# Kernel optimization log

Hardware: AMD Instinct MI355X
Metric: run time of the kernel (lower is better)

Reference implementation:

```python
import jax, jax.numpy as jnp
import numpy as np

N, E, H, OUT, NTYPES, EDGE_IN, T = 20000, 160000, 64, 3, 9, 4, 3
NODE_IN = OUT + 1 + NTYPES  # normalized velocity + normalized youngs + one-hot node type


def _mlp(x, w1, b1, w2, b2):
    # 2-layer MLP with ReLU hidden activation (encoder/processor/decoder blocks)
    return jnp.dot(jax.nn.relu(jnp.dot(x, w1) + b1), w2) + b2


def setup_inputs() -> dict:
    key = jax.random.key(0)
    ks = iter(jax.random.split(key, 48))
    nrm = lambda shape, s=1.0: jax.random.normal(next(ks), shape, jnp.float32) * s
    W = 0.05  # small init scale keeps RK4 trajectories numerically tame
    inp = {
        'world_pos': nrm((N, 3)),
        'velocity': nrm((N, 3)) * 0.1,
        'edge_index': jax.random.randint(next(ks), (2, E), 0, N),
        'mesh_edge_attr': nrm((E, EDGE_IN)),
        'youngs': jax.random.uniform(next(ks), (N, 1), jnp.float32) + 0.5,
        'one_hot_node_type': jax.nn.one_hot(jax.random.randint(next(ks), (N,), 0, NTYPES), NTYPES, dtype=jnp.float32),
        'node_type': jax.random.randint(next(ks), (N, 1), 0, 3),
        't_span': jnp.arange(T, dtype=jnp.float32) * 0.1,  # rk4 step_size=0.1 -> one step per interval
        # normalization statistics (stats dict in the torch code)
        'youngs_mean': jnp.full((1,), 1.0, jnp.float32), 'youngs_std': jnp.ones((1,), jnp.float32),
        'mesh_edge_mean': nrm((EDGE_IN,)) * 0.1, 'mesh_edge_std': jnp.ones((EDGE_IN,), jnp.float32),
        'vel_mean': nrm((3,)) * 0.01, 'vel_std': jnp.ones((3,), jnp.float32),
        'acc_mean': nrm((3,)) * 0.01, 'acc_std': jnp.ones((3,), jnp.float32),
        # node encoder
        'w_ne1': nrm((NODE_IN, H), W), 'b_ne1': jnp.zeros((H,), jnp.float32),
        'w_ne2': nrm((H, H), W), 'b_ne2': jnp.zeros((H,), jnp.float32),
        # edge encoder
        'w_ee1': nrm((EDGE_IN, H), W), 'b_ee1': jnp.zeros((H,), jnp.float32),
        'w_ee2': nrm((H, H), W), 'b_ee2': jnp.zeros((H,), jnp.float32),
        # processor edge-update MLP (in: [e, h_src, h_dst])
        'w_em1': nrm((3 * H, H), W), 'b_em1': jnp.zeros((H,), jnp.float32),
        'w_em2': nrm((H, H), W), 'b_em2': jnp.zeros((H,), jnp.float32),
        # processor node-update MLP (in: [h, agg])
        'w_nm1': nrm((2 * H, H), W), 'b_nm1': jnp.zeros((H,), jnp.float32),
        'w_nm2': nrm((H, H), W), 'b_nm2': jnp.zeros((H,), jnp.float32),
        # decoder -> acceleration
        'w_dec1': nrm((H, H), W), 'b_dec1': jnp.zeros((H,), jnp.float32),
        'w_dec2': nrm((H, OUT), W), 'b_dec2': jnp.zeros((OUT,), jnp.float32),
    }
    return inp


def reference(world_pos, velocity, edge_index, mesh_edge_attr, youngs, one_hot_node_type, node_type, t_span,
              youngs_mean, youngs_std, mesh_edge_mean, mesh_edge_std, vel_mean, vel_std, acc_mean, acc_std,
              w_ne1, b_ne1, w_ne2, b_ne2, w_ee1, b_ee1, w_ee2, b_ee2,
              w_em1, b_em1, w_em2, b_em2, w_nm1, b_nm1, w_nm2, b_nm2,
              w_dec1, b_dec1, w_dec2, b_dec2):
    n = world_pos.shape[0]
    other = jnp.concatenate([(youngs - youngs_mean) / youngs_std, one_hot_node_type], axis=-1)  # [N, 10]
    eattr = (mesh_edge_attr - mesh_edge_mean) / mesh_edge_std  # [E, 4] static, normalized once
    src, dst = edge_index[0], edge_index[1]

    def deriv(pos, vel):
        # NeuralODEFunc: encode -> message passing -> decode acceleration
        vn = (vel - vel_mean) / vel_std
        h = _mlp(jnp.concatenate([vn, other], axis=-1), w_ne1, b_ne1, w_ne2, b_ne2)  # [N, H]
        e = _mlp(eattr, w_ee1, b_ee1, w_ee2, b_ee2)  # [E, H]
        # residual GraphNet block: gather endpoint features, update edges, scatter-sum to nodes
        e = e + _mlp(jnp.concatenate([e, h[src], h[dst]], axis=-1), w_em1, b_em1, w_em2, b_em2)
        agg = jax.ops.segment_sum(e, dst, num_segments=n)  # [N, H]
        h = h + _mlp(jnp.concatenate([h, agg], axis=-1), w_nm1, b_nm1, w_nm2, b_nm2)
        acc = _mlp(h, w_dec1, b_dec1, w_dec2, b_dec2) * acc_std + acc_mean  # unnormalize
        return vel, acc  # d(pos)/dt, d(vel)/dt

    def rk4_step(state, dt):
        pos, vel = state
        k1p, k1v = deriv(pos, vel)
        k2p, k2v = deriv(pos + 0.5 * dt * k1p, vel + 0.5 * dt * k1v)
        k3p, k3v = deriv(pos + 0.5 * dt * k2p, vel + 0.5 * dt * k2v)
        k4p, k4v = deriv(pos + dt * k3p, vel + dt * k3v)
        sixth = dt / 6.0
        pos = pos + sixth * (k1p + 2.0 * k2p + 2.0 * k3p + k4p)
        vel = vel + sixth * (k1v + 2.0 * k2v + 2.0 * k3v + k4v)
        return (pos, vel), (pos, vel)

    dts = t_span[1:] - t_span[:-1]  # equals rk4 step_size 0.1 -> one step per interval
    _, (ptraj, vtraj) = jax.lax.scan(rk4_step, (world_pos, velocity), dts)
    pos_out = jnp.concatenate([world_pos[None], ptraj], axis=0)  # [T, N, 3]
    vel_out = jnp.concatenate([velocity[None], vtraj], axis=0)  # [T, N, 3]
    return pos_out, vel_out
```

## Files before the change

### kernel.cpp

```cpp
#include <hip/hip_runtime.h>
#include <hip/hip_bf16.h>

#define NN 20000
#define NE 160000
#define HD 64
#define TT 3

typedef unsigned short ushortx8 __attribute__((ext_vector_type(8)));
typedef float f32x4 __attribute__((ext_vector_type(4)));
typedef __bf16 bf16x8 __attribute__((ext_vector_type(8)));

__device__ __forceinline__ unsigned short f2bf(float f) {
  unsigned int x = __float_as_uint(f);
  unsigned int r = (x + 0x7fffu + ((x >> 16) & 1u)) >> 16;
  return (unsigned short)r;
}
__device__ __forceinline__ float bf2f(unsigned short u) {
  return __uint_as_float(((unsigned int)u) << 16);
}

__global__ __launch_bounds__(256) void k_prep(const float* __restrict__ wp,
    const float* __restrict__ vel, float* __restrict__ PO, float* __restrict__ VO,
    int* __restrict__ counts, int* __restrict__ fill,
    const float* __restrict__ youngs, const float* __restrict__ onehot,
    const float* __restrict__ ym, const float* __restrict__ ys,
    const float* __restrict__ w_ne1, const float* __restrict__ b_ne1, float* __restrict__ h_pre,
    const float* __restrict__ w_em1, const float* __restrict__ w_em2,
    const float* __restrict__ w_nm1, const float* __restrict__ w_nm2,
    const float* __restrict__ w_dec1, const float* __restrict__ w_ne2, const float* __restrict__ w_ee2,
    char* __restrict__ w1em, char* __restrict__ w2em, char* __restrict__ wnm1,
    char* __restrict__ wnm2, char* __restrict__ wdec1, char* __restrict__ wne2,
    char* __restrict__ wee2) {
  int idx = blockIdx.x * 256 + threadIdx.x;
  if (idx < NN * 3) { PO[idx] = wp[idx]; VO[idx] = vel[idx]; }
  if (idx < NN) { counts[idx] = 0; fill[idx] = 0; }
  {
    int n = idx >> 6, j = idx & 63;
    float a = b_ne1[j];
    float yn = (youngs[n] - ym[0]) / ys[0];
    a += yn * w_ne1[3 * HD + j];
#pragma unroll
    for (int k = 0; k < 9; k++) a += onehot[n * 9 + k] * w_ne1[(4 + k) * HD + j];
    h_pre[idx] = a;
  }
  int w = idx;
  if (w < 12288) {
    int j = w / 192, k = w % 192;
    *(unsigned short*)(w1em + j * 384 + ((k * 2) ^ ((j & 7) << 4))) = f2bf(w_em1[k * 64 + j]);
    return;
  }
  w -= 12288;
  if (w < 4096) {
    int j = w >> 6, k = w & 63;
    *(unsigned short*)(w2em + j * 128 + ((k * 2) ^ ((j & 7) << 4))) = f2bf(w_em2[k * 64 + j]);
    return;
  }
  w -= 4096;
  if (w < 8192) {
    int j = w >> 7, k = w & 127;
    *(unsigned short*)(wnm1 + j * 256 + ((k * 2) ^ ((j & 7) << 4))) = f2bf(w_nm1[k * 64 + j]);
    return;
  }
  w -= 8192;
  if (w < 4096) {
    int j = w >> 6, k = w & 63;
    *(unsigned short*)(wnm2 + j * 128 + ((k * 2) ^ ((j & 7) << 4))) = f2bf(w_nm2[k * 64 + j]);
    return;
  }
  w -= 4096;
  if (w < 4096) {
    int j = w >> 6, k = w & 63;
    *(unsigned short*)(wdec1 + j * 128 + ((k * 2) ^ ((j & 7) << 4))) = f2bf(w_dec1[k * 64 + j]);
    return;
  }
  w -= 4096;
  if (w < 4096) {
    int j = w >> 6, k = w & 63;
    *(unsigned short*)(wne2 + j * 128 + ((k * 2) ^ ((j & 7) << 4))) = f2bf(w_ne2[k * 64 + j]);
    return;
  }
  w -= 4096;
  if (w < 4096) {
    int j = w >> 6, k = w & 63;
    *(unsigned short*)(wee2 + j * 128 + ((k * 2) ^ ((j & 7) << 4))) = f2bf(w_ee2[k * 64 + j]);
    return;
  }
}

__global__ __launch_bounds__(256) void k_edge_enc_mfma(const float* __restrict__ eattr,
    const float* __restrict__ emean, const float* __restrict__ estd,
    const float* __restrict__ w_ee1, const float* __restrict__ b_ee1,
    const char* __restrict__ wee2sw, const float* __restrict__ b_ee2,
    char* __restrict__ eenc_sw) {
  __shared__ __align__(16) char s_w2[64 * 128];
  __shared__ __align__(16) char s_hid[64 * 128];
  __shared__ float s_w1[4 * 64], s_b1[64], s_b2[64], s_m[4], s_s[4];
  int tid = threadIdx.x, e0b = blockIdx.x * 64;
  for (int c = tid; c < 512; c += 256) ((ushortx8*)s_w2)[c] = ((const ushortx8*)wee2sw)[c];
  if (tid < 256) s_w1[tid] = w_ee1[tid];
  if (tid < 64) { s_b1[tid] = b_ee1[tid]; s_b2[tid] = b_ee2[tid]; }
  if (tid < 4) { s_m[tid] = emean[tid]; s_s[tid] = estd[tid]; }
  __syncthreads();
  int lane = tid & 63, wv = tid >> 6, l15 = lane & 15, lq = lane >> 4, csub = lq * 8;
  int row_l = wv * 16 + l15, rsw = (l15 & 7) << 4;
  int erow = e0b + row_l;
  float4 at = ((const float4*)eattr)[erow];
  float x0 = (at.x - s_m[0]) / s_s[0];
  float x1 = (at.y - s_m[1]) / s_s[1];
  float x2 = (at.z - s_m[2]) / s_s[2];
  float x3 = (at.w - s_m[3]) / s_s[3];
#pragma unroll 4
  for (int i = 0; i < 16; i++) {
    int rl = wv * 16 + i;
    float y0 = __shfl(x0, i), y1 = __shfl(x1, i), y2 = __shfl(x2, i), y3 = __shfl(x3, i);
    float a = s_b1[lane] + y0 * s_w1[lane] + y1 * s_w1[64 + lane] + y2 * s_w1[128 + lane] + y3 * s_w1[192 + lane];
    *(unsigned short*)(s_hid + rl * 128 + ((lane * 2) ^ ((rl & 7) << 4))) = f2bf(fmaxf(a, 0.f));
  }
  f32x4 acc[4];
#pragma unroll
  for (int n = 0; n < 4; n++) {
    float bv = s_b2[n * 16 + l15];
#pragma unroll
    for (int i = 0; i < 4; i++) acc[n][i] = bv;
  }
#pragma unroll
  for (int kk = 0; kk < 2; kk++) {
    ushortx8 au = *(const ushortx8*)(s_hid + row_l * 128 + (((kk * 32 + csub) * 2) ^ rsw));
    bf16x8 av = __builtin_bit_cast(bf16x8, au);
#pragma unroll
    for (int n = 0; n < 4; n++) {
      int j = n * 16 + l15;
      ushortx8 bu = *(const ushortx8*)(s_w2 + j * 128 + (((kk * 32 + csub) * 2) ^ ((j & 7) << 4)));
      acc[n] = __builtin_amdgcn_mfma_f32_16x16x32_bf16(av, __builtin_bit_cast(bf16x8, bu), acc[n], 0, 0, 0);
    }
  }
#pragma unroll
  for (int n = 0; n < 4; n++) {
#pragma unroll
    for (int i = 0; i < 4; i++) {
      int r = wv * 16 + lq * 4 + i, col = n * 16 + l15;
      *(unsigned short*)(s_hid + r * 128 + ((col * 2) ^ ((r & 7) << 4))) = f2bf(acc[n][i]);
    }
  }
  ushortx8 q0 = *(const ushortx8*)(s_hid + row_l * 128 + lq * 32);
  ushortx8 q1 = *(const ushortx8*)(s_hid + row_l * 128 + lq * 32 + 16);
  *(ushortx8*)(eenc_sw + (size_t)erow * 128 + lq * 32) = q0;
  *(ushortx8*)(eenc_sw + (size_t)erow * 128 + lq * 32 + 16) = q1;
}

__global__ __launch_bounds__(256) void k_count(const int* __restrict__ eidx, int* __restrict__ counts) {
  int e = blockIdx.x * 256 + threadIdx.x;
  if (e < NE) atomicAdd(&counts[eidx[NE + e]], 1);
}

#define SCAN_NB ((NN + 255) / 256)
__global__ __launch_bounds__(256) void k_scanA(const int* __restrict__ counts,
    int* __restrict__ row_ptr, int* __restrict__ bsums) {
  __shared__ int tmp[256];
  int tid = threadIdx.x;
  int g = blockIdx.x * 256 + tid;
  int v = (g < NN) ? counts[g] : 0;
  tmp[tid] = v;
  __syncthreads();
#pragma unroll
  for (int off = 1; off < 256; off <<= 1) {
    int t = (tid >= off) ? tmp[tid - off] : 0;
    __syncthreads();
    tmp[tid] += t;
    __syncthreads();
  }
  if (g < NN) row_ptr[g] = tmp[tid] - v;
  if (tid == 255) bsums[blockIdx.x] = tmp[255];
}

__global__ __launch_bounds__(128) void k_scanB(int* __restrict__ bsums) {
  __shared__ int tmp[128];
  int tid = threadIdx.x;
  int v = (tid < SCAN_NB) ? bsums[tid] : 0;
  tmp[tid] = v;
  __syncthreads();
#pragma unroll
  for (int off = 1; off < 128; off <<= 1) {
    int t = (tid >= off) ? tmp[tid - off] : 0;
    __syncthreads();
    tmp[tid] += t;
    __syncthreads();
  }
  if (tid < SCAN_NB) bsums[tid] = tmp[tid] - v;
}

__global__ __launch_bounds__(256) void k_scanC(int* __restrict__ row_ptr, const int* __restrict__ bsums) {
  int g = blockIdx.x * 256 + threadIdx.x;
  if (g < NN) row_ptr[g] += bsums[blockIdx.x];
  if (g == 0) row_ptr[NN] = NE;
}

__global__ __launch_bounds__(256) void k_place(const int* __restrict__ eidx,
    const int* __restrict__ row_ptr, int* __restrict__ fill, int* __restrict__ slot) {
  int e = blockIdx.x * 256 + threadIdx.x;
  if (e >= NE) return;
  int d = eidx[NE + e];
  int f = atomicAdd(&fill[d], 1);
  slot[e] = row_ptr[d] + f;
}

__global__ __launch_bounds__(256) void k_enc_mfma(const float* __restrict__ vel,
    const float* __restrict__ vmean, const float* __restrict__ vstd,
    const float* __restrict__ w_ne1, const float* __restrict__ h_pre,
    const char* __restrict__ wne2sw, const float* __restrict__ b_ne2,
    float* __restrict__ h, unsigned short* __restrict__ h_bf) {
  __shared__ __align__(16) char s_w2[64 * 128];
  __shared__ __align__(16) char s_hid[64 * 128];
  __shared__ float s_w1[3 * 64], s_b2[64], s_vm[3], s_vs[3];
  int tid = threadIdx.x, n0b = blockIdx.x * 64;
  for (int c = tid; c < 512; c += 256) ((ushortx8*)s_w2)[c] = ((const ushortx8*)wne2sw)[c];
  if (tid < 192) s_w1[tid] = w_ne1[tid];
  if (tid < 64) s_b2[tid] = b_ne2[tid];
  if (tid < 3) { s_vm[tid] = vmean[tid]; s_vs[tid] = vstd[tid]; }
  __syncthreads();
  int lane = tid & 63, wv = tid >> 6, l15 = lane & 15, lq = lane >> 4, csub = lq * 8;
#pragma unroll 4
  for (int i = 0; i < 16; i++) {
    int rl = wv * 16 + i, node = n0b + rl;
    float hv = 0.f;
    if (node < NN) {
      float v0 = (vel[node * 3 + 0] - s_vm[0]) / s_vs[0];
      float v1 = (vel[node * 3 + 1] - s_vm[1]) / s_vs[1];
      float v2 = (vel[node * 3 + 2] - s_vm[2]) / s_vs[2];
      float a = h_pre[(size_t)node * 64 + lane] + v0 * s_w1[lane] + v1 * s_w1[64 + lane] + v2 * s_w1[128 + lane];
      hv = fmaxf(a, 0.f);
    }
    *(unsigned short*)(s_hid + rl * 128 + ((lane * 2) ^ ((rl & 7) << 4))) = f2bf(hv);
  }
  int row_l = wv * 16 + l15, rsw = (l15 & 7) << 4;
  f32x4 acc[4];
#pragma unroll
  for (int n = 0; n < 4; n++) {
    float bv = s_b2[n * 16 + l15];
#pragma unroll
    for (int i = 0; i < 4; i++) acc[n][i] = bv;
  }
#pragma unroll
  for (int kk = 0; kk < 2; kk++) {
    ushortx8 au = *(const ushortx8*)(s_hid + row_l * 128 + (((kk * 32 + csub) * 2) ^ rsw));
    bf16x8 av = __builtin_bit_cast(bf16x8, au);
#pragma unroll
    for (int n = 0; n < 4; n++) {
      int j = n * 16 + l15;
      ushortx8 bu = *(const ushortx8*)(s_w2 + j * 128 + (((kk * 32 + csub) * 2) ^ ((j & 7) << 4)));
      acc[n] = __builtin_amdgcn_mfma_f32_16x16x32_bf16(av, __builtin_bit_cast(bf16x8, bu), acc[n], 0, 0, 0);
    }
  }
#pragma unroll
  for (int n = 0; n < 4; n++) {
#pragma unroll
    for (int i = 0; i < 4; i++) {
      int r = wv * 16 + lq * 4 + i, rowg = n0b + r, col = n * 16 + l15;
      if (rowg < NN) h[(size_t)rowg * 64 + col] = acc[n][i];
      *(unsigned short*)(s_hid + r * 128 + ((col * 2) ^ ((r & 7) << 4))) = f2bf(acc[n][i]);
    }
  }
  int noderow = n0b + row_l;
  if (noderow < NN) {
    ushortx8 q0 = *(const ushortx8*)(s_hid + row_l * 128 + ((lq * 32) ^ rsw));
    ushortx8 q1 = *(const ushortx8*)(s_hid + row_l * 128 + ((lq * 32 + 16) ^ rsw));
    ushortx8* op = (ushortx8*)(h_bf + (size_t)noderow * 64);
    op[lq * 2] = q0;
    op[lq * 2 + 1] = q1;
  }
}

#define EDGE_GRID 1024
__global__ __launch_bounds__(256, 4) void k_edge_mfma(
    const int* __restrict__ eidx, const int* __restrict__ slot,
    const unsigned short* __restrict__ h_bf, const char* __restrict__ eenc_sw,
    const char* __restrict__ w1sw, const char* __restrict__ w2sw,
    const float* __restrict__ b_em1, const float* __restrict__ b_em2,
    unsigned short* __restrict__ emsg) {
  __shared__ __align__(16) char s_w1[64 * 384];
  __shared__ __align__(16) char s_w2[64 * 128];
  __shared__ __align__(16) char s_eh[64 * 128];
  int tid = threadIdx.x;
  int lane = tid & 63, wv = tid >> 6, l15 = lane & 15, lq = lane >> 4, csub = lq * 8;
  int erow_loc = wv * 16 + l15;
  int rsw = (l15 & 7) << 4;
  for (int c = tid; c < 1536; c += 256) ((ushortx8*)s_w1)[c] = ((const ushortx8*)w1sw)[c];
  for (int c = tid; c < 512; c += 256) ((ushortx8*)s_w2)[c] = ((const ushortx8*)w2sw)[c];
  float bv1[4], bv2[4];
#pragma unroll
  for (int n = 0; n < 4; n++) { bv1[n] = b_em1[n * 16 + l15]; bv2[n] = b_em2[n * 16 + l15]; }

  const int NT = NE / 64;
  ushortx8 stg0, stg1;
  {
    const ushortx8* src = (const ushortx8*)(eenc_sw + (size_t)blockIdx.x * 64 * 128);
    stg0 = src[tid];
    stg1 = src[tid + 256];
  }
  for (int t = blockIdx.x; t < NT; t += EDGE_GRID) {
    int e0b = t * 64;
    int eg = e0b + erow_loc;
    int sidx = eidx[eg], didx = eidx[NE + eg], sl = slot[eg];
    const ushortx8* hs = (const ushortx8*)(h_bf + (size_t)sidx * HD);
    const ushortx8* hd = (const ushortx8*)(h_bf + (size_t)didx * HD);
    ushortx8 a2 = hs[lq];
    ushortx8 a3 = hs[4 + lq];
    ushortx8 a4 = hd[lq];
    ushortx8 a5 = hd[4 + lq];
    __syncthreads();
    ((ushortx8*)s_eh)[tid] = stg0;
    ((ushortx8*)s_eh)[tid + 256] = stg1;
    __syncthreads();
    int tn = t + EDGE_GRID;
    if (tn < NT) {
      const ushortx8* srcn = (const ushortx8*)(eenc_sw + (size_t)tn * 64 * 128);
      stg0 = srcn[tid];
      stg1 = srcn[tid + 256];
    }
    ushortx8 a0 = *(const ushortx8*)(s_eh + erow_loc * 128 + ((csub * 2) ^ rsw));
    ushortx8 a1 = *(const ushortx8*)(s_eh + erow_loc * 128 + ((64 + csub * 2) ^ rsw));
    f32x4 acc[4];
#pragma unroll
    for (int n = 0; n < 4; n++) {
#pragma unroll
      for (int i = 0; i < 4; i++) acc[n][i] = bv1[n];
    }
    ushortx8 af[6] = {a0, a1, a2, a3, a4, a5};
#pragma unroll
    for (int kk = 0; kk < 6; kk++) {
      bf16x8 av = __builtin_bit_cast(bf16x8, af[kk]);
#pragma unroll
      for (int n = 0; n < 4; n++) {
        int j = n * 16 + l15;
        ushortx8 bu = *(const ushortx8*)(s_w1 + j * 384 + (((kk * 32 + csub) * 2) ^ ((j & 7) << 4)));
        acc[n] = __builtin_amdgcn_mfma_f32_16x16x32_bf16(av, __builtin_bit_cast(bf16x8, bu), acc[n], 0, 0, 0);
      }
    }
    f32x4 acc2[4];
#pragma unroll
    for (int n = 0; n < 4; n++) {
#pragma unroll
      for (int i = 0; i < 4; i++) {
        int r = wv * 16 + lq * 4 + i, col = n * 16 + l15;
        unsigned short ev = *(const unsigned short*)(s_eh + r * 128 + ((col * 2) ^ ((r & 7) << 4)));
        acc2[n][i] = bv2[n] + bf2f(ev);
      }
    }
#pragma unroll
    for (int n = 0; n < 4; n++) {
#pragma unroll
      for (int i = 0; i < 4; i++) {
        int r = wv * 16 + lq * 4 + i, col = n * 16 + l15;
        *(unsigned short*)(s_eh + r * 128 + ((col * 2) ^ ((r & 7) << 4))) = f2bf(fmaxf(acc[n][i], 0.f));
      }
    }
#pragma unroll
    for (int kk = 0; kk < 2; kk++) {
      ushortx8 au = *(const ushortx8*)(s_eh + erow_loc * 128 + (((kk * 32 + csub) * 2) ^ rsw));
      bf16x8 av = __builtin_bit_cast(bf16x8, au);
#pragma unroll
      for (int n = 0; n < 4; n++) {
        int j = n * 16 + l15;
        ushortx8 bu = *(const ushortx8*)(s_w2 + j * 128 + (((kk * 32 + csub) * 2) ^ ((j & 7) << 4)));
        acc2[n] = __builtin_amdgcn_mfma_f32_16x16x32_bf16(av, __builtin_bit_cast(bf16x8, bu), acc2[n], 0, 0, 0);
      }
    }
#pragma unroll
    for (int n = 0; n < 4; n++) {
#pragma unroll
      for (int i = 0; i < 4; i++) {
        int r = wv * 16 + lq * 4 + i, col = n * 16 + l15;
        *(unsigned short*)(s_eh + r * 128 + ((col * 2) ^ ((r & 7) << 4))) = f2bf(acc2[n][i]);
      }
    }
    ushortx8 q0 = *(const ushortx8*)(s_eh + erow_loc * 128 + ((lq * 32) ^ rsw));
    ushortx8 q1 = *(const ushortx8*)(s_eh + erow_loc * 128 + ((lq * 32 + 16) ^ rsw));
    ushortx8* op = (ushortx8*)(emsg + (size_t)sl * HD);
    op[lq * 2] = q0;
    op[lq * 2 + 1] = q1;
  }
}

__global__ __launch_bounds__(128) void k_upd_enc(
    const int* __restrict__ row_ptr, const unsigned short* __restrict__ emsg,
    float* __restrict__ hbuf, unsigned short* __restrict__ h_bf,
    const char* __restrict__ wnm1sw, const char* __restrict__ wnm2sw,
    const char* __restrict__ wdec1sw, const char* __restrict__ wne2sw,
    const float* __restrict__ b_nm1, const float* __restrict__ b_nm2,
    const float* __restrict__ b_dec1, const float* __restrict__ b_dec2,
    const float* __restrict__ w_dec2, const float* __restrict__ amean, const float* __restrict__ astd,
    const float* __restrict__ w_ne1, const float* __restrict__ h_pre,
    const float* __restrict__ b_ne2, const float* __restrict__ vmean, const float* __restrict__ vstd,
    const float* __restrict__ tspan, int s, int k, int do_enc,
    const float* __restrict__ V0, float* __restrict__ vacc, float* __restrict__ pacc,
    const float* __restrict__ pos_prev, float* __restrict__ pos_next, float* __restrict__ vel_next) {
  __shared__ __align__(16) char s_w1[64 * 256];
  __shared__ __align__(16) char s_w2[64 * 128];
  __shared__ __align__(16) char s_wd1[64 * 128];
  __shared__ __align__(16) char s_w2e[64 * 128];
  __shared__ __align__(16) char s_ah[32 * 128];
  __shared__ float s_b1[64], s_b2[64], s_bd1[64], s_be2[64], s_wd2[192], s_w1e[192];
  __shared__ float s_vm[3], s_vs[3];
  int tid = threadIdx.x, n0b = blockIdx.x * 32;
  for (int c = tid; c < 1024; c += 128) ((ushortx8*)s_w1)[c] = ((const ushortx8*)wnm1sw)[c];
  for (int c = tid; c < 512; c += 128) ((ushortx8*)s_w2)[c] = ((const ushortx8*)wnm2sw)[c];
  for (int c = tid; c < 512; c += 128) ((ushortx8*)s_wd1)[c] = ((const ushortx8*)wdec1sw)[c];
  for (int c = tid; c < 512; c += 128) ((ushortx8*)s_w2e)[c] = ((const ushortx8*)wne2sw)[c];
  if (tid < 64) { s_b1[tid] = b_nm1[tid]; s_b2[tid] = b_nm2[tid]; s_bd1[tid] = b_dec1[tid]; s_be2[tid] = b_ne2[tid]; }
  for (int i = tid; i < 192; i += 128) { s_wd2[i] = w_dec2[i]; s_w1e[i] = w_ne1[i]; }
  if (tid < 3) { s_vm[tid] = vmean[tid]; s_vs[tid] = vstd[tid]; }

  int lane = tid & 63, wv = tid >> 6, l15 = lane & 15, lq = lane >> 4, csub = lq * 8;
  int row_l = wv * 16 + l15, rsw = (l15 & 7) << 4;
  int noderow = n0b + row_l;
  int ncl = noderow < NN ? noderow : NN - 1;
  ushortx8 afh0 = *(const ushortx8*)(h_bf + (size_t)ncl * 64 + csub);
  ushortx8 afh1 = *(const ushortx8*)(h_bf + (size_t)ncl * 64 + 32 + csub);

  int arow = lane >> 3, ag = lane & 7;
#pragma unroll
  for (int p = 0; p < 2; p++) {
    int rl = wv * 16 + p * 8 + arow, node = n0b + rl;
    float sm[8] = {0.f, 0.f, 0.f, 0.f, 0.f, 0.f, 0.f, 0.f};
    if (node < NN) {
      int b = row_ptr[node], e = row_ptr[node + 1];
      for (int r = b; r < e; r++) {
        ushortx8 u = *(const ushortx8*)(emsg + (size_t)r * HD + ag * 8);
#pragma unroll
        for (int j = 0; j < 8; j++) sm[j] += bf2f(u[j]);
      }
    }
    ushortx8 u;
#pragma unroll
    for (int j = 0; j < 8; j++) u[j] = f2bf(sm[j]);
    *(ushortx8*)(s_ah + rl * 128 + ((ag * 16) ^ ((rl & 7) << 4))) = u;
  }
  __syncthreads();

  f32x4 acc[4];
#pragma unroll
  for (int n = 0; n < 4; n++) {
    float bv = s_b1[n * 16 + l15];
#pragma unroll
    for (int i = 0; i < 4; i++) acc[n][i] = bv;
  }
  ushortx8 af[4];
  af[0] = afh0; af[1] = afh1;
  af[2] = *(const ushortx8*)(s_ah + row_l * 128 + ((csub * 2) ^ rsw));
  af[3] = *(const ushortx8*)(s_ah + row_l * 128 + (((32 + csub) * 2) ^ rsw));
#pragma unroll
  for (int kk = 0; kk < 4; kk++) {
    bf16x8 av = __builtin_bit_cast(bf16x8, af[kk]);
#pragma unroll
    for (int n = 0; n < 4; n++) {
      int j = n * 16 + l15;
      ushortx8 bu = *(const ushortx8*)(s_w1 + j * 256 + (((kk * 32 + csub) * 2) ^ ((j & 7) << 4)));
      acc[n] = __builtin_amdgcn_mfma_f32_16x16x32_bf16(av, __builtin_bit_cast(bf16x8, bu), acc[n], 0, 0, 0);
    }
  }
#pragma unroll
  for (int n = 0; n < 4; n++) {
#pragma unroll
    for (int i = 0; i < 4; i++) {
      int r = wv * 16 + lq * 4 + i, col = n * 16 + l15;
      *(unsigned short*)(s_ah + r * 128 + ((col * 2) ^ ((r & 7) << 4))) = f2bf(fmaxf(acc[n][i], 0.f));
    }
  }
  f32x4 acc2[4];
#pragma unroll
  for (int n = 0; n < 4; n++) {
#pragma unroll
    for (int i = 0; i < 4; i++) {
      int r = wv * 16 + lq * 4 + i, col = n * 16 + l15;
      int rg = n0b + r; int rgc = rg < NN ? rg : NN - 1;
      acc2[n][i] = s_b2[col] + hbuf[(size_t)rgc * 64 + col];
    }
  }
#pragma unroll
  for (int kk = 0; kk < 2; kk++) {
    ushortx8 au = *(const ushortx8*)(s_ah + row_l * 128 + (((kk * 32 + csub) * 2) ^ rsw));
    bf16x8 av = __builtin_bit_cast(bf16x8, au);
#pragma unroll
    for (int n = 0; n < 4; n++) {
      int j = n * 16 + l15;
      ushortx8 bu = *(const ushortx8*)(s_w2 + j * 128 + (((kk * 32 + csub) * 2) ^ ((j & 7) << 4)));
      acc2[n] = __builtin_amdgcn_mfma_f32_16x16x32_bf16(av, __builtin_bit_cast(bf16x8, bu), acc2[n], 0, 0, 0);
    }
  }
#pragma unroll
  for (int n = 0; n < 4; n++) {
#pragma unroll
    for (int i = 0; i < 4; i++) {
      int r = wv * 16 + lq * 4 + i, col = n * 16 + l15;
      *(unsigned short*)(s_ah + r * 128 + ((col * 2) ^ ((r & 7) << 4))) = f2bf(acc2[n][i]);
    }
  }
  f32x4 acc3[4];
#pragma unroll
  for (int n = 0; n < 4; n++) {
    float bv = s_bd1[n * 16 + l15];
#pragma unroll
    for (int i = 0; i < 4; i++) acc3[n][i] = bv;
  }
#pragma unroll
  for (int kk = 0; kk < 2; kk++) {
    ushortx8 au = *(const ushortx8*)(s_ah + row_l * 128 + (((kk * 32 + csub) * 2) ^ rsw));
    bf16x8 av = __builtin_bit_cast(bf16x8, au);
#pragma unroll
    for (int n = 0; n < 4; n++) {
      int j = n * 16 + l15;
      ushortx8 bu = *(const ushortx8*)(s_wd1 + j * 128 + (((kk * 32 + csub) * 2) ^ ((j & 7) << 4)));
      acc3[n] = __builtin_amdgcn_mfma_f32_16x16x32_bf16(av, __builtin_bit_cast(bf16x8, bu), acc3[n], 0, 0, 0);
    }
  }
#pragma unroll
  for (int n = 0; n < 4; n++) {
#pragma unroll
    for (int i = 0; i < 4; i++) {
      int r = wv * 16 + lq * 4 + i, col = n * 16 + l15;
      *(unsigned short*)(s_ah + r * 128 + ((col * 2) ^ ((r & 7) << 4))) = f2bf(fmaxf(acc3[n][i], 0.f));
    }
  }
  ushortx8 u0 = *(const ushortx8*)(s_ah + row_l * 128 + ((lq * 32) ^ rsw));
  ushortx8 u1 = *(const ushortx8*)(s_ah + row_l * 128 + ((lq * 32 + 16) ^ rsw));
  float p[3] = {0.f, 0.f, 0.f};
#pragma unroll
  for (int i = 0; i < 8; i++) {
    float x0 = bf2f(u0[i]), x1 = bf2f(u1[i]);
    int c0 = lq * 16 + i, c1 = lq * 16 + 8 + i;
#pragma unroll
    for (int t = 0; t < 3; t++) p[t] += x0 * s_wd2[c0 * 3 + t] + x1 * s_wd2[c1 * 3 + t];
  }
#pragma unroll
  for (int t = 0; t < 3; t++) {
    p[t] += __shfl_xor(p[t], 16);
    p[t] += __shfl_xor(p[t], 32);
  }
  float dt = tspan[s + 1] - tspan[s];
  float o[3];
#pragma unroll
  for (int t = 0; t < 3; t++) o[t] = (p[t] + b_dec2[t]) * astd[t] + amean[t];
  const float ck = (k == 2) ? 1.0f : 0.5f;
  float vs[3] = {0.f, 0.f, 0.f};
  if (noderow < NN) {
    if (lq == 0) {
#pragma unroll
      for (int t = 0; t < 3; t++) {
        float v0v = V0[noderow * 3 + t];
        float wk = (k == 0 || k == 3) ? 1.f : 2.f;
        float va = (k == 0) ? o[t] : vacc[noderow * 3 + t] + wk * o[t];
        if (k < 3) {
          vacc[noderow * 3 + t] = va;
          vs[t] = v0v + ck * dt * o[t];
        } else {
          float vn = v0v + (dt / 6.f) * va;
          vel_next[noderow * 3 + t] = vn;
          vs[t] = vn;
        }
      }
    } else if (lq == 1) {
#pragma unroll
      for (int t = 0; t < 3; t++) {
        if (k < 3) {
          float v0v = V0[noderow * 3 + t];
          float vst = v0v + ck * dt * o[t];
          float pa;
          if (k == 0) pa = v0v + 2.f * vst;
          else pa = pacc[noderow * 3 + t] + ((k == 1) ? 2.f : 1.f) * vst;
          pacc[noderow * 3 + t] = pa;
        } else {
          pos_next[noderow * 3 + t] = pos_prev[noderow * 3 + t] + (dt / 6.f) * pacc[noderow * 3 + t];
        }
      }
    }
  }
  if (do_enc) {
    for (int i = 0; i < 16; i++) {
      int rl = wv * 16 + i, node = n0b + rl;
      float v0s = __shfl(vs[0], i);
      float v1s = __shfl(vs[1], i);
      float v2s = __shfl(vs[2], i);
      float hv = 0.f;
      if (node < NN) {
        float vn0 = (v0s - s_vm[0]) / s_vs[0];
        float vn1 = (v1s - s_vm[1]) / s_vs[1];
        float vn2 = (v2s - s_vm[2]) / s_vs[2];
        float a = h_pre[(size_t)node * 64 + lane] + vn0 * s_w1e[lane] + vn1 * s_w1e[64 + lane] + vn2 * s_w1e[128 + lane];
        hv = fmaxf(a, 0.f);
      }
      *(unsigned short*)(s_ah + rl * 128 + ((lane * 2) ^ ((rl & 7) << 4))) = f2bf(hv);
    }
    f32x4 ae[4];
#pragma unroll
    for (int n = 0; n < 4; n++) {
      float bv = s_be2[n * 16 + l15];
#pragma unroll
      for (int i = 0; i < 4; i++) ae[n][i] = bv;
    }
#pragma unroll
    for (int kk = 0; kk < 2; kk++) {
      ushortx8 au = *(const ushortx8*)(s_ah + row_l * 128 + (((kk * 32 + csub) * 2) ^ rsw));
      bf16x8 av = __builtin_bit_cast(bf16x8, au);
#pragma unroll
      for (int n = 0; n < 4; n++) {
        int j = n * 16 + l15;
        ushortx8 bu = *(const ushortx8*)(s_w2e + j * 128 + (((kk * 32 + csub) * 2) ^ ((j & 7) << 4)));
        ae[n] = __builtin_amdgcn_mfma_f32_16x16x32_bf16(av, __builtin_bit_cast(bf16x8, bu), ae[n], 0, 0, 0);
      }
    }
#pragma unroll
    for (int n = 0; n < 4; n++) {
#pragma unroll
      for (int i = 0; i < 4; i++) {
        int r = wv * 16 + lq * 4 + i, rowg = n0b + r, col = n * 16 + l15;
        if (rowg < NN) hbuf[(size_t)rowg * 64 + col] = ae[n][i];
        *(unsigned short*)(s_ah + r * 128 + ((col * 2) ^ ((r & 7) << 4))) = f2bf(ae[n][i]);
      }
    }
    if (noderow < NN) {
      ushortx8 q0 = *(const ushortx8*)(s_ah + row_l * 128 + ((lq * 32) ^ rsw));
      ushortx8 q1 = *(const ushortx8*)(s_ah + row_l * 128 + ((lq * 32 + 16) ^ rsw));
      ushortx8* op = (ushortx8*)(h_bf + (size_t)noderow * 64);
      op[lq * 2] = q0;
      op[lq * 2 + 1] = q1;
    }
  }
}

extern "C" void kernel_launch(void* const* d_in, const int* in_sizes, int n_in,
                              void* d_out, int out_size, void* d_ws, size_t ws_size,
                              hipStream_t stream) {
  (void)in_sizes; (void)n_in; (void)out_size; (void)ws_size;
  const float* world_pos = (const float*)d_in[0];
  const float* velocity  = (const float*)d_in[1];
  const int*   eidx      = (const int*)d_in[2];
  const float* eattr     = (const float*)d_in[3];
  const float* youngs    = (const float*)d_in[4];
  const float* onehot    = (const float*)d_in[5];
  const float* tspan     = (const float*)d_in[7];
  const float* ym        = (const float*)d_in[8];
  const float* ys        = (const float*)d_in[9];
  const float* emean     = (const float*)d_in[10];
  const float* estd      = (const float*)d_in[11];
  const float* vmean     = (const float*)d_in[12];
  const float* vstd      = (const float*)d_in[13];
  const float* amean     = (const float*)d_in[14];
  const float* astd      = (const float*)d_in[15];
  const float* w_ne1 = (const float*)d_in[16]; const float* b_ne1 = (const float*)d_in[17];
  const float* w_ne2 = (const float*)d_in[18]; const float* b_ne2 = (const float*)d_in[19];
  const float* w_ee1 = (const float*)d_in[20]; const float* b_ee1 = (const float*)d_in[21];
  const float* w_ee2 = (const float*)d_in[22]; const float* b_ee2 = (const float*)d_in[23];
  const float* w_em1 = (const float*)d_in[24]; const float* b_em1 = (const float*)d_in[25];
  const float* w_em2 = (const float*)d_in[26]; const float* b_em2 = (const float*)d_in[27];
  const float* w_nm1 = (const float*)d_in[28]; const float* b_nm1 = (const float*)d_in[29];
  const float* w_nm2 = (const float*)d_in[30]; const float* b_nm2 = (const float*)d_in[31];
  const float* w_dec1 = (const float*)d_in[32]; const float* b_dec1 = (const float*)d_in[33];
  const float* w_dec2 = (const float*)d_in[34]; const float* b_dec2 = (const float*)d_in[35];

  char* ws = (char*)d_ws;
  float* h_pre  = (float*)ws; ws += (size_t)NN * HD * 4;
  float* hbuf   = (float*)ws; ws += (size_t)NN * HD * 4;
  char* eenc_sw = ws; ws += (size_t)NE * 128;
  unsigned short* emsg_bf = (unsigned short*)ws; ws += (size_t)NE * HD * 2;
  unsigned short* h_bf    = (unsigned short*)ws; ws += (size_t)NN * HD * 2;
  char* w1em  = ws; ws += 64 * 384;
  char* w2em  = ws; ws += 64 * 128;
  char* wnm1s = ws; ws += 64 * 256;
  char* wnm2s = ws; ws += 64 * 128;
  char* wdec1s = ws; ws += 64 * 128;
  char* wne2s = ws; ws += 64 * 128;
  char* wee2s = ws; ws += 64 * 128;
  float* vacc = (float*)ws; ws += (size_t)NN * 3 * 4;
  float* pacc = (float*)ws; ws += (size_t)NN * 3 * 4;
  int* counts  = (int*)ws; ws += (size_t)NN * 4;
  int* fill    = (int*)ws; ws += (size_t)NN * 4;
  int* slot    = (int*)ws; ws += (size_t)NE * 4;
  int* row_ptr = (int*)ws; ws += (size_t)(NN + 1) * 4;
  int* bsums   = (int*)ws; ws += (size_t)128 * 4;

  float* PO = (float*)d_out;
  float* VO = PO + (size_t)TT * NN * 3;

  k_prep<<<(NN * HD) / 256, 256, 0, stream>>>(world_pos, velocity, PO, VO, counts, fill,
                                              youngs, onehot, ym, ys, w_ne1, b_ne1, h_pre,
                                              w_em1, w_em2, w_nm1, w_nm2, w_dec1, w_ne2, w_ee2,
                                              w1em, w2em, wnm1s, wnm2s, wdec1s, wne2s, wee2s);
  k_edge_enc_mfma<<<NE / 64, 256, 0, stream>>>(eattr, emean, estd, w_ee1, b_ee1, wee2s, b_ee2, eenc_sw);
  k_count<<<NE / 256, 256, 0, stream>>>(eidx, counts);
  k_scanA<<<SCAN_NB, 256, 0, stream>>>(counts, row_ptr, bsums);
  k_scanB<<<1, 128, 0, stream>>>(bsums);
  k_scanC<<<SCAN_NB, 256, 0, stream>>>(row_ptr, bsums);
  k_place<<<NE / 256, 256, 0, stream>>>(eidx, row_ptr, fill, slot);

  const int NBLK_ENC = (NN + 63) / 64;
  const int NBLK_UPD = (NN + 31) / 32;
  k_enc_mfma<<<NBLK_ENC, 256, 0, stream>>>(velocity, vmean, vstd, w_ne1, h_pre, wne2s, b_ne2, hbuf, h_bf);

  for (int s = 0; s < TT - 1; s++) {
    const float* V0 = VO + (size_t)s * NN * 3;
    const float* pos_prev = PO + (size_t)s * NN * 3;
    float* pos_next = PO + (size_t)(s + 1) * NN * 3;
    float* vel_next = VO + (size_t)(s + 1) * NN * 3;
    for (int k = 0; k < 4; k++) {
      k_edge_mfma<<<EDGE_GRID, 256, 0, stream>>>(eidx, slot, h_bf, eenc_sw, w1em, w2em,
                                                 b_em1, b_em2, emsg_bf);
      int do_enc = !(s == TT - 2 && k == 3);
      k_upd_enc<<<NBLK_UPD, 128, 0, stream>>>(row_ptr, emsg_bf, hbuf, h_bf,
                                              wnm1s, wnm2s, wdec1s, wne2s,
                                              b_nm1, b_nm2, b_dec1, b_dec2, w_dec2, amean, astd,
                                              w_ne1, h_pre, b_ne2, vmean, vstd,
                                              tspan, s, k, do_enc,
                                              V0, vacc, pacc, pos_prev, pos_next, vel_next);
    }
  }
}
```

Baseline: 422.5 us.

## Prefetch gathered node rows in edge kernel, fuse count, widen update blocks

The edge kernel now prefetches the next tile's source and destination node features, indices and slots during the current tile's MFMA work, extending the existing software pipeline beyond the edge-encoding staging. This aims to hide the latency of the random gathers. The edge-count atomic is folded into the edge encoder kernel, removing one launch. The node update kernel moves from 128 to 256 threads per block with 64 nodes per block, which halves the number of blocks and raises register pressure from the extra prefetch state.

New measurement: 414.3 us. No clear change (-1.9%).

```diff
diff --git a/kernel.cpp b/kernel.cpp
--- a/kernel.cpp
+++ b/kernel.cpp
@@ -91,7 +91,7 @@
     const float* __restrict__ emean, const float* __restrict__ estd,
     const float* __restrict__ w_ee1, const float* __restrict__ b_ee1,
     const char* __restrict__ wee2sw, const float* __restrict__ b_ee2,
-    char* __restrict__ eenc_sw) {
+    char* __restrict__ eenc_sw, const int* __restrict__ eidx, int* __restrict__ counts) {
   __shared__ __align__(16) char s_w2[64 * 128];
   __shared__ __align__(16) char s_hid[64 * 128];
   __shared__ float s_w1[4 * 64], s_b1[64], s_b2[64], s_m[4], s_s[4];
@@ -104,6 +104,7 @@
   int lane = tid & 63, wv = tid >> 6, l15 = lane & 15, lq = lane >> 4, csub = lq * 8;
   int row_l = wv * 16 + l15, rsw = (l15 & 7) << 4;
   int erow = e0b + row_l;
+  if (lq == 0) atomicAdd(&counts[eidx[NE + erow]], 1);
   float4 at = ((const float4*)eattr)[erow];
   float x0 = (at.x - s_m[0]) / s_s[0];
   float x1 = (at.y - s_m[1]) / s_s[1];
@@ -146,11 +147,6 @@
   ushortx8 q1 = *(const ushortx8*)(s_hid + row_l * 128 + lq * 32 + 16);
   *(ushortx8*)(eenc_sw + (size_t)erow * 128 + lq * 32) = q0;
   *(ushortx8*)(eenc_sw + (size_t)erow * 128 + lq * 32 + 16) = q1;
-}
-
-__global__ __launch_bounds__(256) void k_count(const int* __restrict__ eidx, int* __restrict__ counts) {
-  int e = blockIdx.x * 256 + threadIdx.x;
-  if (e < NE) atomicAdd(&counts[eidx[NE + e]], 1);
 }
 
 #define SCAN_NB ((NN + 255) / 256)
@@ -291,31 +287,40 @@
   for (int n = 0; n < 4; n++) { bv1[n] = b_em1[n * 16 + l15]; bv2[n] = b_em2[n * 16 + l15]; }
 
   const int NT = NE / 64;
-  ushortx8 stg0, stg1;
+  int t = blockIdx.x;
+  ushortx8 stg0, stg1, a2, a3, a4, a5;
+  int sl;
   {
-    const ushortx8* src = (const ushortx8*)(eenc_sw + (size_t)blockIdx.x * 64 * 128);
+    const ushortx8* src = (const ushortx8*)(eenc_sw + (size_t)t * 64 * 128);
     stg0 = src[tid];
     stg1 = src[tid + 256];
-  }
-  for (int t = blockIdx.x; t < NT; t += EDGE_GRID) {
-    int e0b = t * 64;
-    int eg = e0b + erow_loc;
-    int sidx = eidx[eg], didx = eidx[NE + eg], sl = slot[eg];
+    int eg = t * 64 + erow_loc;
+    int sidx = eidx[eg], didx = eidx[NE + eg];
+    sl = slot[eg];
     const ushortx8* hs = (const ushortx8*)(h_bf + (size_t)sidx * HD);
     const ushortx8* hd = (const ushortx8*)(h_bf + (size_t)didx * HD);
-    ushortx8 a2 = hs[lq];
-    ushortx8 a3 = hs[4 + lq];
-    ushortx8 a4 = hd[lq];
-    ushortx8 a5 = hd[4 + lq];
+    a2 = hs[lq]; a3 = hs[4 + lq]; a4 = hd[lq]; a5 = hd[4 + lq];
+  }
+  while (t < NT) {
     __syncthreads();
     ((ushortx8*)s_eh)[tid] = stg0;
     ((ushortx8*)s_eh)[tid + 256] = stg1;
     __syncthreads();
     int tn = t + EDGE_GRID;
+    ushortx8 stg0n, stg1n, a2n, a3n, a4n, a5n;
+    int sln = 0;
     if (tn < NT) {
       const ushortx8* srcn = (const ushortx8*)(eenc_sw + (size_t)tn * 64 * 128);
-      stg0 = srcn[tid];
-      stg1 = srcn[tid + 256];
+      stg0n = srcn[tid];
+      stg1n = srcn[tid + 256];
+      int egn = tn * 64 + erow_loc;
+      int sidxn = eidx[egn], didxn = eidx[NE + egn];
+      sln = slot[egn];
+      const ushortx8* hsn = (const ushortx8*)(h_bf + (size_t)sidxn * HD);
+      const ushortx8* hdn = (const ushortx8*)(h_bf + (size_t)didxn * HD);
+      a2n = hsn[lq]; a3n = hsn[4 + lq]; a4n = hdn[lq]; a5n = hdn[4 + lq];
+    } else {
+      stg0n = stg0; stg1n = stg1; a2n = a2; a3n = a3; a4n = a4; a5n = a5;
     }
     ushortx8 a0 = *(const ushortx8*)(s_eh + erow_loc * 128 + ((csub * 2) ^ rsw));
     ushortx8 a1 = *(const ushortx8*)(s_eh + erow_loc * 128 + ((64 + csub * 2) ^ rsw));
@@ -378,10 +383,14 @@
     ushortx8* op = (ushortx8*)(emsg + (size_t)sl * HD);
     op[lq * 2] = q0;
     op[lq * 2 + 1] = q1;
-  }
-}
-
-__global__ __launch_bounds__(128) void k_upd_enc(
+    t = tn;
+    stg0 = stg0n; stg1 = stg1n;
+    a2 = a2n; a3 = a3n; a4 = a4n; a5 = a5n;
+    sl = sln;
+  }
+}
+
+__global__ __launch_bounds__(256) void k_upd_enc(
     const int* __restrict__ row_ptr, const unsigned short* __restrict__ emsg,
     float* __restrict__ hbuf, unsigned short* __restrict__ h_bf,
     const char* __restrict__ wnm1sw, const char* __restrict__ wnm2sw,
@@ -398,16 +407,16 @@
   __shared__ __align__(16) char s_w2[64 * 128];
   __shared__ __align__(16) char s_wd1[64 * 128];
   __shared__ __align__(16) char s_w2e[64 * 128];
-  __shared__ __align__(16) char s_ah[32 * 128];
+  __shared__ __align__(16) char s_ah[64 * 128];
   __shared__ float s_b1[64], s_b2[64], s_bd1[64], s_be2[64], s_wd2[192], s_w1e[192];
   __shared__ float s_vm[3], s_vs[3];
-  int tid = threadIdx.x, n0b = blockIdx.x * 32;
-  for (int c = tid; c < 1024; c += 128) ((ushortx8*)s_w1)[c] = ((const ushortx8*)wnm1sw)[c];
-  for (int c = tid; c < 512; c += 128) ((ushortx8*)s_w2)[c] = ((const ushortx8*)wnm2sw)[c];
-  for (int c = tid; c < 512; c += 128) ((ushortx8*)s_wd1)[c] = ((const ushortx8*)wdec1sw)[c];
-  for (int c = tid; c < 512; c += 128) ((ushortx8*)s_w2e)[c] = ((const ushortx8*)wne2sw)[c];
+  int tid = threadIdx.x, n0b = blockIdx.x * 64;
+  for (int c = tid; c < 1024; c += 256) ((ushortx8*)s_w1)[c] = ((const ushortx8*)wnm1sw)[c];
+  for (int c = tid; c < 512; c += 256) ((ushortx8*)s_w2)[c] = ((const ushortx8*)wnm2sw)[c];
+  for (int c = tid; c < 512; c += 256) ((ushortx8*)s_wd1)[c] = ((const ushortx8*)wdec1sw)[c];
+  for (int c = tid; c < 512; c += 256) ((ushortx8*)s_w2e)[c] = ((const ushortx8*)wne2sw)[c];
   if (tid < 64) { s_b1[tid] = b_nm1[tid]; s_b2[tid] = b_nm2[tid]; s_bd1[tid] = b_dec1[tid]; s_be2[tid] = b_ne2[tid]; }
-  for (int i = tid; i < 192; i += 128) { s_wd2[i] = w_dec2[i]; s_w1e[i] = w_ne1[i]; }
+  if (tid < 192) { s_wd2[tid] = w_dec2[tid]; s_w1e[tid] = w_ne1[tid]; }
   if (tid < 3) { s_vm[tid] = vmean[tid]; s_vs[tid] = vstd[tid]; }
 
   int lane = tid & 63, wv = tid >> 6, l15 = lane & 15, lq = lane >> 4, csub = lq * 8;
@@ -685,16 +694,15 @@
                                               youngs, onehot, ym, ys, w_ne1, b_ne1, h_pre,
                                               w_em1, w_em2, w_nm1, w_nm2, w_dec1, w_ne2, w_ee2,
                                               w1em, w2em, wnm1s, wnm2s, wdec1s, wne2s, wee2s);
-  k_edge_enc_mfma<<<NE / 64, 256, 0, stream>>>(eattr, emean, estd, w_ee1, b_ee1, wee2s, b_ee2, eenc_sw);
-  k_count<<<NE / 256, 256, 0, stream>>>(eidx, counts);
+  k_edge_enc_mfma<<<NE / 64, 256, 0, stream>>>(eattr, emean, estd, w_ee1, b_ee1, wee2s, b_ee2,
+                                               eenc_sw, eidx, counts);
   k_scanA<<<SCAN_NB, 256, 0, stream>>>(counts, row_ptr, bsums);
   k_scanB<<<1, 128, 0, stream>>>(bsums);
   k_scanC<<<SCAN_NB, 256, 0, stream>>>(row_ptr, bsums);
   k_place<<<NE / 256, 256, 0, stream>>>(eidx, row_ptr, fill, slot);
 
-  const int NBLK_ENC = (NN + 63) / 64;
-  const int NBLK_UPD = (NN + 31) / 32;
-  k_enc_mfma<<<NBLK_ENC, 256, 0, stream>>>(velocity, vmean, vstd, w_ne1, h_pre, wne2s, b_ne2, hbuf, h_bf);
+  const int NBLK = (NN + 63) / 64;
+  k_enc_mfma<<<NBLK, 256, 0, stream>>>(velocity, vmean, vstd, w_ne1, h_pre, wne2s, b_ne2, hbuf, h_bf);
 
   for (int s = 0; s < TT - 1; s++) {
     const float* V0 = VO + (size_t)s * NN * 3;
@@ -705,12 +713,12 @@
       k_edge_mfma<<<EDGE_GRID, 256, 0, stream>>>(eidx, slot, h_bf, eenc_sw, w1em, w2em,
                                                  b_em1, b_em2, emsg_bf);
       int do_enc = !(s == TT - 2 && k == 3);
-      k_upd_enc<<<NBLK_UPD, 128, 0, stream>>>(row_ptr, emsg_bf, hbuf, h_bf,
-                                              wnm1s, wnm2s, wdec1s, wne2s,
-                                              b_nm1, b_nm2, b_dec1, b_dec2, w_dec2, amean, astd,
-                                              w_ne1, h_pre, b_ne2, vmean, vstd,
-                                              tspan, s, k, do_enc,
-                                              V0, vacc, pacc, pos_prev, pos_next, vel_next);
-    }
-  }
-}
+      k_upd_enc<<<NBLK, 256, 0, stream>>>(row_ptr, emsg_bf, hbuf, h_bf,
+                                          wnm1s, wnm2s, wdec1s, wne2s,
+                                          b_nm1, b_nm2, b_dec1, b_dec2, w_dec2, amean, astd,
+                                          w_ne1, h_pre, b_ne2, vmean, vstd,
+                                          tspan, s, k, do_enc,
+                                          V0, vacc, pacc, pos_prev, pos_next, vel_next);
+    }
+  }
+}
```

## Drop fp32 node buffers, fuse edge counting, widen node-update blocks to 64 rows

Applied to the files above, without the earlier changes.

Stores the precomputed encoder input and the node hidden state only in bf16. This removes the fp32 h_pre and hbuf buffers and their global reads and writes. The separate k_count kernel is folded into the edge-encoder kernel as an atomic per edge. The node update/encode kernel now runs 256 threads on 64 nodes per block instead of 128 threads on 32, with an added barrier before the shared tile is reused. The residual path now reads bf16 h, which lowers precision across RK4 stages.

Result: faster. 393.7 us, median of 2 (-6.8%).

```diff
diff --git a/kernel.cpp b/kernel.cpp
--- a/kernel.cpp
+++ b/kernel.cpp
@@ -24,7 +24,8 @@
     int* __restrict__ counts, int* __restrict__ fill,
     const float* __restrict__ youngs, const float* __restrict__ onehot,
     const float* __restrict__ ym, const float* __restrict__ ys,
-    const float* __restrict__ w_ne1, const float* __restrict__ b_ne1, float* __restrict__ h_pre,
+    const float* __restrict__ w_ne1, const float* __restrict__ b_ne1,
+    unsigned short* __restrict__ h_pre_bf,
     const float* __restrict__ w_em1, const float* __restrict__ w_em2,
     const float* __restrict__ w_nm1, const float* __restrict__ w_nm2,
     const float* __restrict__ w_dec1, const float* __restrict__ w_ne2, const float* __restrict__ w_ee2,
@@ -41,7 +42,7 @@
     a += yn * w_ne1[3 * HD + j];
 #pragma unroll
     for (int k = 0; k < 9; k++) a += onehot[n * 9 + k] * w_ne1[(4 + k) * HD + j];
-    h_pre[idx] = a;
+    h_pre_bf[idx] = f2bf(a);
   }
   int w = idx;
   if (w < 12288) {
@@ -91,7 +92,7 @@
     const float* __restrict__ emean, const float* __restrict__ estd,
     const float* __restrict__ w_ee1, const float* __restrict__ b_ee1,
     const char* __restrict__ wee2sw, const float* __restrict__ b_ee2,
-    char* __restrict__ eenc_sw) {
+    char* __restrict__ eenc_sw, const int* __restrict__ eidx, int* __restrict__ counts) {
   __shared__ __align__(16) char s_w2[64 * 128];
   __shared__ __align__(16) char s_hid[64 * 128];
   __shared__ float s_w1[4 * 64], s_b1[64], s_b2[64], s_m[4], s_s[4];
@@ -104,6 +105,7 @@
   int lane = tid & 63, wv = tid >> 6, l15 = lane & 15, lq = lane >> 4, csub = lq * 8;
   int row_l = wv * 16 + l15, rsw = (l15 & 7) << 4;
   int erow = e0b + row_l;
+  if (lq == 0) atomicAdd(&counts[eidx[NE + erow]], 1);
   float4 at = ((const float4*)eattr)[erow];
   float x0 = (at.x - s_m[0]) / s_s[0];
   float x1 = (at.y - s_m[1]) / s_s[1];
@@ -148,11 +150,6 @@
   *(ushortx8*)(eenc_sw + (size_t)erow * 128 + lq * 32 + 16) = q1;
 }
 
-__global__ __launch_bounds__(256) void k_count(const int* __restrict__ eidx, int* __restrict__ counts) {
-  int e = blockIdx.x * 256 + threadIdx.x;
-  if (e < NE) atomicAdd(&counts[eidx[NE + e]], 1);
-}
-
 #define SCAN_NB ((NN + 255) / 256)
 __global__ __launch_bounds__(256) void k_scanA(const int* __restrict__ counts,
     int* __restrict__ row_ptr, int* __restrict__ bsums) {
@@ -206,9 +203,9 @@
 
 __global__ __launch_bounds__(256) void k_enc_mfma(const float* __restrict__ vel,
     const float* __restrict__ vmean, const float* __restrict__ vstd,
-    const float* __restrict__ w_ne1, const float* __restrict__ h_pre,
+    const float* __restrict__ w_ne1, const unsigned short* __restrict__ h_pre_bf,
     const char* __restrict__ wne2sw, const float* __restrict__ b_ne2,
-    float* __restrict__ h, unsigned short* __restrict__ h_bf) {
+    unsigned short* __restrict__ h_bf) {
   __shared__ __align__(16) char s_w2[64 * 128];
   __shared__ __align__(16) char s_hid[64 * 128];
   __shared__ float s_w1[3 * 64], s_b2[64], s_vm[3], s_vs[3];
@@ -227,7 +224,7 @@
       float v0 = (vel[node * 3 + 0] - s_vm[0]) / s_vs[0];
       float v1 = (vel[node * 3 + 1] - s_vm[1]) / s_vs[1];
       float v2 = (vel[node * 3 + 2] - s_vm[2]) / s_vs[2];
-      float a = h_pre[(size_t)node * 64 + lane] + v0 * s_w1[lane] + v1 * s_w1[64 + lane] + v2 * s_w1[128 + lane];
+      float a = bf2f(h_pre_bf[(size_t)node * 64 + lane]) + v0 * s_w1[lane] + v1 * s_w1[64 + lane] + v2 * s_w1[128 + lane];
       hv = fmaxf(a, 0.f);
     }
     *(unsigned short*)(s_hid + rl * 128 + ((lane * 2) ^ ((rl & 7) << 4))) = f2bf(hv);
@@ -255,8 +252,7 @@
   for (int n = 0; n < 4; n++) {
 #pragma unroll
     for (int i = 0; i < 4; i++) {
-      int r = wv * 16 + lq * 4 + i, rowg = n0b + r, col = n * 16 + l15;
-      if (rowg < NN) h[(size_t)rowg * 64 + col] = acc[n][i];
+      int r = wv * 16 + lq * 4 + i, col = n * 16 + l15;
       *(unsigned short*)(s_hid + r * 128 + ((col * 2) ^ ((r & 7) << 4))) = f2bf(acc[n][i]);
     }
   }
@@ -381,15 +377,15 @@
   }
 }
 
-__global__ __launch_bounds__(128) void k_upd_enc(
+__global__ __launch_bounds__(256) void k_upd_enc(
     const int* __restrict__ row_ptr, const unsigned short* __restrict__ emsg,
-    float* __restrict__ hbuf, unsigned short* __restrict__ h_bf,
+    unsigned short* __restrict__ h_bf,
     const char* __restrict__ wnm1sw, const char* __restrict__ wnm2sw,
     const char* __restrict__ wdec1sw, const char* __restrict__ wne2sw,
     const float* __restrict__ b_nm1, const float* __restrict__ b_nm2,
     const float* __restrict__ b_dec1, const float* __restrict__ b_dec2,
     const float* __restrict__ w_dec2, const float* __restrict__ amean, const float* __restrict__ astd,
-    const float* __restrict__ w_ne1, const float* __restrict__ h_pre,
+    const float* __restrict__ w_ne1, const unsigned short* __restrict__ h_pre_bf,
     const float* __restrict__ b_ne2, const float* __restrict__ vmean, const float* __restrict__ vstd,
     const float* __restrict__ tspan, int s, int k, int do_enc,
     const float* __restrict__ V0, float* __restrict__ vacc, float* __restrict__ pacc,
@@ -398,16 +394,16 @@
   __shared__ __align__(16) char s_w2[64 * 128];
   __shared__ __align__(16) char s_wd1[64 * 128];
   __shared__ __align__(16) char s_w2e[64 * 128];
-  __shared__ __align__(16) char s_ah[32 * 128];
+  __shared__ __align__(16) char s_ah[64 * 128];
   __shared__ float s_b1[64], s_b2[64], s_bd1[64], s_be2[64], s_wd2[192], s_w1e[192];
   __shared__ float s_vm[3], s_vs[3];
-  int tid = threadIdx.x, n0b = blockIdx.x * 32;
-  for (int c = tid; c < 1024; c += 128) ((ushortx8*)s_w1)[c] = ((const ushortx8*)wnm1sw)[c];
-  for (int c = tid; c < 512; c += 128) ((ushortx8*)s_w2)[c] = ((const ushortx8*)wnm2sw)[c];
-  for (int c = tid; c < 512; c += 128) ((ushortx8*)s_wd1)[c] = ((const ushortx8*)wdec1sw)[c];
-  for (int c = tid; c < 512; c += 128) ((ushortx8*)s_w2e)[c] = ((const ushortx8*)wne2sw)[c];
+  int tid = threadIdx.x, n0b = blockIdx.x * 64;
+  for (int c = tid; c < 1024; c += 256) ((ushortx8*)s_w1)[c] = ((const ushortx8*)wnm1sw)[c];
+  for (int c = tid; c < 512; c += 256) ((ushortx8*)s_w2)[c] = ((const ushortx8*)wnm2sw)[c];
+  for (int c = tid; c < 512; c += 256) ((ushortx8*)s_wd1)[c] = ((const ushortx8*)wdec1sw)[c];
+  for (int c = tid; c < 512; c += 256) ((ushortx8*)s_w2e)[c] = ((const ushortx8*)wne2sw)[c];
   if (tid < 64) { s_b1[tid] = b_nm1[tid]; s_b2[tid] = b_nm2[tid]; s_bd1[tid] = b_dec1[tid]; s_be2[tid] = b_ne2[tid]; }
-  for (int i = tid; i < 192; i += 128) { s_wd2[i] = w_dec2[i]; s_w1e[i] = w_ne1[i]; }
+  if (tid < 192) { s_wd2[tid] = w_dec2[tid]; s_w1e[tid] = w_ne1[tid]; }
   if (tid < 3) { s_vm[tid] = vmean[tid]; s_vs[tid] = vstd[tid]; }
 
   int lane = tid & 63, wv = tid >> 6, l15 = lane & 15, lq = lane >> 4, csub = lq * 8;
@@ -473,7 +469,7 @@
     for (int i = 0; i < 4; i++) {
       int r = wv * 16 + lq * 4 + i, col = n * 16 + l15;
       int rg = n0b + r; int rgc = rg < NN ? rg : NN - 1;
-      acc2[n][i] = s_b2[col] + hbuf[(size_t)rgc * 64 + col];
+      acc2[n][i] = s_b2[col] + bf2f(h_bf[(size_t)rgc * 64 + col]);
     }
   }
 #pragma unroll
@@ -585,7 +581,7 @@
         float vn0 = (v0s - s_vm[0]) / s_vs[0];
         float vn1 = (v1s - s_vm[1]) / s_vs[1];
         float vn2 = (v2s - s_vm[2]) / s_vs[2];
-        float a = h_pre[(size_t)node * 64 + lane] + vn0 * s_w1e[lane] + vn1 * s_w1e[64 + lane] + vn2 * s_w1e[128 + lane];
+        float a = bf2f(h_pre_bf[(size_t)node * 64 + lane]) + vn0 * s_w1e[lane] + vn1 * s_w1e[64 + lane] + vn2 * s_w1e[128 + lane];
         hv = fmaxf(a, 0.f);
       }
       *(unsigned short*)(s_ah + rl * 128 + ((lane * 2) ^ ((rl & 7) << 4))) = f2bf(hv);
@@ -608,12 +604,12 @@
         ae[n] = __builtin_amdgcn_mfma_f32_16x16x32_bf16(av, __builtin_bit_cast(bf16x8, bu), ae[n], 0, 0, 0);
       }
     }
+    __syncthreads();
 #pragma unroll
     for (int n = 0; n < 4; n++) {
 #pragma unroll
       for (int i = 0; i < 4; i++) {
-        int r = wv * 16 + lq * 4 + i, rowg = n0b + r, col = n * 16 + l15;
-        if (rowg < NN) hbuf[(size_t)rowg * 64 + col] = ae[n][i];
+        int r = wv * 16 + lq * 4 + i, col = n * 16 + l15;
         *(unsigned short*)(s_ah + r * 128 + ((col * 2) ^ ((r & 7) << 4))) = f2bf(ae[n][i]);
       }
     }
@@ -658,8 +654,7 @@
   const float* w_dec2 = (const float*)d_in[34]; const float* b_dec2 = (const float*)d_in[35];
 
   char* ws = (char*)d_ws;
-  float* h_pre  = (float*)ws; ws += (size_t)NN * HD * 4;
-  float* hbuf   = (float*)ws; ws += (size_t)NN * HD * 4;
+  unsigned short* h_pre_bf = (unsigned short*)ws; ws += (size_t)NN * HD * 2;
   char* eenc_sw = ws; ws += (size_t)NE * 128;
   unsigned short* emsg_bf = (unsigned short*)ws; ws += (size_t)NE * HD * 2;
   unsigned short* h_bf    = (unsigned short*)ws; ws += (size_t)NN * HD * 2;
@@ -682,19 +677,18 @@
   float* VO = PO + (size_t)TT * NN * 3;
 
   k_prep<<<(NN * HD) / 256, 256, 0, stream>>>(world_pos, velocity, PO, VO, counts, fill,
-                                              youngs, onehot, ym, ys, w_ne1, b_ne1, h_pre,
+                                              youngs, onehot, ym, ys, w_ne1, b_ne1, h_pre_bf,
                                               w_em1, w_em2, w_nm1, w_nm2, w_dec1, w_ne2, w_ee2,
                                               w1em, w2em, wnm1s, wnm2s, wdec1s, wne2s, wee2s);
-  k_edge_enc_mfma<<<NE / 64, 256, 0, stream>>>(eattr, emean, estd, w_ee1, b_ee1, wee2s, b_ee2, eenc_sw);
-  k_count<<<NE / 256, 256, 0, stream>>>(eidx, counts);
+  k_edge_enc_mfma<<<NE / 64, 256, 0, stream>>>(eattr, emean, estd, w_ee1, b_ee1, wee2s, b_ee2,
+                                               eenc_sw, eidx, counts);
   k_scanA<<<SCAN_NB, 256, 0, stream>>>(counts, row_ptr, bsums);
   k_scanB<<<1, 128, 0, stream>>>(bsums);
   k_scanC<<<SCAN_NB, 256, 0, stream>>>(row_ptr, bsums);
   k_place<<<NE / 256, 256, 0, stream>>>(eidx, row_ptr, fill, slot);
 
-  const int NBLK_ENC = (NN + 63) / 64;
-  const int NBLK_UPD = (NN + 31) / 32;
-  k_enc_mfma<<<NBLK_ENC, 256, 0, stream>>>(velocity, vmean, vstd, w_ne1, h_pre, wne2s, b_ne2, hbuf, h_bf);
+  const int NBLK = (NN + 63) / 64;
+  k_enc_mfma<<<NBLK, 256, 0, stream>>>(velocity, vmean, vstd, w_ne1, h_pre_bf, wne2s, b_ne2, h_bf);
 
   for (int s = 0; s < TT - 1; s++) {
     const float* V0 = VO + (size_t)s * NN * 3;
@@ -705,12 +699,12 @@
       k_edge_mfma<<<EDGE_GRID, 256, 0, stream>>>(eidx, slot, h_bf, eenc_sw, w1em, w2em,
                                                  b_em1, b_em2, emsg_bf);
       int do_enc = !(s == TT - 2 && k == 3);
-      k_upd_enc<<<NBLK_UPD, 128, 0, stream>>>(row_ptr, emsg_bf, hbuf, h_bf,
-                                              wnm1s, wnm2s, wdec1s, wne2s,
-                                              b_nm1, b_nm2, b_dec1, b_dec2, w_dec2, amean, astd,
-                                              w_ne1, h_pre, b_ne2, vmean, vstd,
-                                              tspan, s, k, do_enc,
-                                              V0, vacc, pacc, pos_prev, pos_next, vel_next);
-    }
-  }
-}
+      k_upd_enc<<<NBLK, 256, 0, stream>>>(row_ptr, emsg_bf, h_bf,
+                                          wnm1s, wnm2s, wdec1s, wne2s,
+                                          b_nm1, b_nm2, b_dec1, b_dec2, w_dec2, amean, astd,
+                                          w_ne1, h_pre_bf, b_ne2, vmean, vstd,
+                                          tspan, s, k, do_enc,
+                                          V0, vacc, pacc, pos_prev, pos_next, vel_next);
+    }
+  }
+}
```
